# Optimization experiments

Hardware: AMD Instinct MI355X
Metric: run time of the kernel (lower is better)

The kernel has to match this reference:

```python
import jax, jax.numpy as jnp
import numpy as np

# PlatonicConv (graph mode, attention=True, use_key=True): tetrahedron group G=12
G = 12
H_EFF = 2          # num_heads // G = 24 // 12
HEAD_D = 16        # embed_dim_g // H_EFF = (384//12) // 2
GH = G * H_EFF     # 24
IN_C = 384
EMB = 384
OUT_C = 384
N_GRAPHS = 32
NODES_PER_GRAPH = 64
N = N_GRAPHS * NODES_PER_GRAPH   # 2048
SPATIAL = 3


def _fc_edges():
    # fully-connected edges within each graph (batch[src]==batch[dst]), incl. self loops
    n = NODES_PER_GRAPH
    offs = np.arange(N_GRAPHS, dtype=np.int32) * n
    gs, gd = np.meshgrid(np.arange(n, dtype=np.int32), np.arange(n, dtype=np.int32), indexing='ij')
    src = (offs[:, None] + gs.reshape(-1)[None, :]).reshape(-1)
    dst = (offs[:, None] + gd.reshape(-1)[None, :]).reshape(-1)
    return jnp.asarray(src), jnp.asarray(dst)


def setup_inputs() -> dict:
    key = jax.random.key(0)
    ks = jax.random.split(key, 12)
    sw = 1.0 / np.sqrt(IN_C)
    x = jax.random.normal(ks[0], (N, IN_C), jnp.float32)
    pos = jax.random.normal(ks[1], (N, SPATIAL), jnp.float32)
    Wq = jax.random.normal(ks[2], (IN_C, EMB), jnp.float32) * sw
    bq = jnp.zeros((EMB,), jnp.float32)
    Wk = jax.random.normal(ks[3], (IN_C, EMB), jnp.float32) * sw
    bk = jnp.zeros((EMB,), jnp.float32)
    Wv = jax.random.normal(ks[4], (IN_C, EMB), jnp.float32) * sw
    bv = jnp.zeros((EMB,), jnp.float32)
    Wo = jax.random.normal(ks[5], (EMB, OUT_C), jnp.float32) * (1.0 / np.sqrt(EMB))
    bo = jnp.zeros((OUT_C,), jnp.float32)
    # RoPE frequencies: freq_sigma=1.0, random init, per spatial dim / head / half-dim
    rope_freqs = jax.random.normal(ks[6], (SPATIAL, H_EFF, HEAD_D // 2), jnp.float32)
    src, dst = _fc_edges()
    return {"x": x, "pos": pos, "Wq": Wq, "bq": bq, "Wk": Wk, "bk": bk,
            "Wv": Wv, "bv": bv, "Wo": Wo, "bo": bo, "rope_freqs": rope_freqs,
            "src": src, "dst": dst}


def _rope(t, pos, freqs):
    # t: [N, G, H, D]; pos: [N, 3]; freqs: [3, H, D//2]
    theta = jnp.einsum('ns,shf->nhf', pos, freqs)            # [N, H, D/2]
    cos = jnp.cos(theta)[:, None, :, :]                      # broadcast over G
    sin = jnp.sin(theta)[:, None, :, :]
    tr = t.reshape(t.shape[:-1] + (HEAD_D // 2, 2))
    t1, t2 = tr[..., 0], tr[..., 1]
    rot = jnp.stack([t1 * cos - t2 * sin, t1 * sin + t2 * cos], axis=-1)
    return rot.reshape(t.shape)


def reference(x, pos, Wq, bq, Wk, bk, Wv, bv, Wo, bo, rope_freqs, src, dst):
    n = x.shape[0]
    q = (x @ Wq + bq).reshape(n, G, H_EFF, HEAD_D)
    k = (x @ Wk + bk).reshape(n, G, H_EFF, HEAD_D)
    v = (x @ Wv + bv).reshape(n, G, H_EFF, HEAD_D)
    q = _rope(q, pos, rope_freqs)
    k = _rope(k, pos, rope_freqs)
    qf = q.reshape(n, GH, HEAD_D)
    kf = k.reshape(n, GH, HEAD_D)
    vf = v.reshape(n, GH, HEAD_D)
    # gather by edge index
    q_src = qf[src]                                          # [E, GH, D]
    k_dst = kf[dst]
    v_dst = vf[dst]
    scores = jnp.sum(q_src * k_dst, axis=-1) * (HEAD_D ** -0.5)  # [E, GH]
    # scatter softmax over edges grouped by src node (per group-head)
    m = jax.ops.segment_max(scores, src, num_segments=n)     # [N, GH]
    ex = jnp.exp(scores - m[src])
    den = jax.ops.segment_sum(ex, src, num_segments=n)
    a = ex / den[src]                                        # [E, GH]
    out = jax.ops.segment_sum(a[..., None] * v_dst, src, num_segments=n)  # [N, GH, D]
    out = out.reshape(n, GH * HEAD_D)
    return out @ Wo + bo
```

## Files before the change

### kernel.cpp

```cpp
#include <hip/hip_runtime.h>


#define NNODES   2048
#define EMBD     384
#define QKV_LD   1152
#define NGRAPHS  32
#define NPG      64
#define GHEADS   24
#define HDIM     16

typedef __attribute__((ext_vector_type(8))) short short8;
typedef __attribute__((ext_vector_type(4))) float f32x4;

__device__ __forceinline__ short f2bf(float f) {
    unsigned u = __builtin_bit_cast(unsigned, f);
    u += 0x7FFFu + ((u >> 16) & 1u);
    return (short)(u >> 16);
}

__global__ __launch_bounds__(256) void gemm_bias_kernel(
    const float* __restrict__ A, int lda,
    const float* __restrict__ B0, const float* __restrict__ B1,
    const float* __restrict__ B2, int ldb,
    const float* __restrict__ bias0, const float* __restrict__ bias1,
    const float* __restrict__ bias2,
    float* __restrict__ C, int ldc, int K)
{
    __shared__ __align__(16) short As[64 * 40];
    __shared__ __align__(16) short Bs[64 * 40];

    const int tid = threadIdx.x;
    const int m0 = blockIdx.x * 64;
    const int n0 = blockIdx.y * 64;

    const int seg = n0 / 384;
    const float* __restrict__ B    = (seg == 0) ? B0 : (seg == 1) ? B1 : B2;
    const float* __restrict__ bias = (seg == 0) ? bias0 : (seg == 1) ? bias1 : bias2;
    const int nloc = n0 - seg * 384;

    const int r  = tid >> 2;
    const int kq = (tid & 3) * 8;

    const int lane = tid & 63;
    const int w    = tid >> 6;
    const int wr   = (w >> 1) * 32;
    const int wc   = (w & 1) * 32;
    const int fr   = lane & 15;
    const int ko   = (lane >> 4) * 8;

    f32x4 acc[2][2];
    #pragma unroll
    for (int i = 0; i < 2; ++i)
        #pragma unroll
        for (int j = 0; j < 2; ++j)
            acc[i][j] = (f32x4){0.f, 0.f, 0.f, 0.f};

    for (int kt = 0; kt < K; kt += 32) {
        {
            const f32x4* ap = reinterpret_cast<const f32x4*>(
                A + (size_t)(m0 + r) * lda + kt + kq);
            f32x4 a0 = ap[0];
            f32x4 a1 = ap[1];
            short8 av;
            av[0] = f2bf(a0[0]); av[1] = f2bf(a0[1]);
            av[2] = f2bf(a0[2]); av[3] = f2bf(a0[3]);
            av[4] = f2bf(a1[0]); av[5] = f2bf(a1[1]);
            av[6] = f2bf(a1[2]); av[7] = f2bf(a1[3]);
            *reinterpret_cast<short8*>(&As[r * 40 + kq]) = av;
        }
        {
            const float* bp = B + (size_t)(kt + kq) * ldb + nloc + r;
            short8 bv;
            #pragma unroll
            for (int j = 0; j < 8; ++j)
                bv[j] = f2bf(bp[(size_t)j * ldb]);
            *reinterpret_cast<short8*>(&Bs[r * 40 + kq]) = bv;
        }
        __syncthreads();

        short8 af0 = *reinterpret_cast<const short8*>(&As[(wr + fr) * 40 + ko]);
        short8 af1 = *reinterpret_cast<const short8*>(&As[(wr + 16 + fr) * 40 + ko]);
        short8 bf0 = *reinterpret_cast<const short8*>(&Bs[(wc + fr) * 40 + ko]);
        short8 bf1 = *reinterpret_cast<const short8*>(&Bs[(wc + 16 + fr) * 40 + ko]);

        acc[0][0] = __builtin_amdgcn_mfma_f32_16x16x32_bf16(af0, bf0, acc[0][0], 0, 0, 0);
        acc[0][1] = __builtin_amdgcn_mfma_f32_16x16x32_bf16(af0, bf1, acc[0][1], 0, 0, 0);
        acc[1][0] = __builtin_amdgcn_mfma_f32_16x16x32_bf16(af1, bf0, acc[1][0], 0, 0, 0);
        acc[1][1] = __builtin_amdgcn_mfma_f32_16x16x32_bf16(af1, bf1, acc[1][1], 0, 0, 0);
        __syncthreads();
    }

    #pragma unroll
    for (int mi = 0; mi < 2; ++mi) {
        #pragma unroll
        for (int ni = 0; ni < 2; ++ni) {
            const int col  = n0 + wc + ni * 16 + fr;
            const float bv = bias[nloc + wc + ni * 16 + fr];
            const int rowb = m0 + wr + mi * 16 + (lane >> 4) * 4;
            #pragma unroll
            for (int rr = 0; rr < 4; ++rr) {
                C[(size_t)(rowb + rr) * ldc + col] = acc[mi][ni][rr] + bv;
            }
        }
    }
}

__global__ __launch_bounds__(64) void attn_kernel(
    const float* __restrict__ qkv,
    const float* __restrict__ pos,
    const float* __restrict__ freqs,
    float* __restrict__ attn_out)
{
    const int blk  = blockIdx.x;
    const int gr   = blk / GHEADS;
    const int gh   = blk - gr * GHEADS;
    const int h    = gh & 1;
    const int lane = threadIdx.x;
    const int n    = gr * NPG + lane;

    const float* rowq = qkv + (size_t)n * QKV_LD + gh * HDIM;
    const float* rowk = rowq + 384;
    const float* rowv = rowq + 768;

    const float p0 = pos[n * 3 + 0], p1 = pos[n * 3 + 1], p2 = pos[n * 3 + 2];
    float cs[8], sn[8];
    #pragma unroll
    for (int f = 0; f < 8; ++f) {
        const float th = p0 * freqs[h * 8 + f]
                       + p1 * freqs[16 + h * 8 + f]
                       + p2 * freqs[32 + h * 8 + f];
        cs[f] = __cosf(th);
        sn[f] = __sinf(th);
    }

    __shared__ float klds[NPG][HDIM];
    __shared__ float vlds[NPG][HDIM];

    float q[HDIM];
    #pragma unroll
    for (int f = 0; f < 8; ++f) {
        const float q1 = rowq[2 * f], q2 = rowq[2 * f + 1];
        q[2 * f]     = q1 * cs[f] - q2 * sn[f];
        q[2 * f + 1] = q1 * sn[f] + q2 * cs[f];
    }
    #pragma unroll
    for (int f = 0; f < 8; ++f) {
        const float k1 = rowk[2 * f], k2 = rowk[2 * f + 1];
        klds[lane][2 * f]     = k1 * cs[f] - k2 * sn[f];
        klds[lane][2 * f + 1] = k1 * sn[f] + k2 * cs[f];
    }
    #pragma unroll
    for (int d = 0; d < HDIM; ++d)
        vlds[lane][d] = rowv[d];
    __syncthreads();

    float sc[NPG];
    #pragma unroll
    for (int j = 0; j < NPG; ++j) {
        float a = 0.f;
        #pragma unroll
        for (int d = 0; d < HDIM; ++d)
            a += q[d] * klds[j][d];
        sc[j] = a * 0.25f;
    }

    float m = sc[0];
    #pragma unroll
    for (int j = 1; j < NPG; ++j) m = fmaxf(m, sc[j]);

    float den = 0.f;
    #pragma unroll
    for (int j = 0; j < NPG; ++j) {
        sc[j] = __expf(sc[j] - m);
        den += sc[j];
    }

    float o[HDIM];
    #pragma unroll
    for (int d = 0; d < HDIM; ++d) o[d] = 0.f;
    #pragma unroll
    for (int j = 0; j < NPG; ++j) {
        const float p = sc[j];
        #pragma unroll
        for (int d = 0; d < HDIM; ++d)
            o[d] += p * vlds[j][d];
    }

    const float inv = 1.0f / den;
    float* outp = attn_out + (size_t)n * EMBD + gh * HDIM;
    #pragma unroll
    for (int d = 0; d < HDIM; ++d)
        outp[d] = o[d] * inv;
}

extern "C" void kernel_launch(void* const* d_in, const int* in_sizes, int n_in,
                              void* d_out, int out_size, void* d_ws, size_t ws_size,
                              hipStream_t stream) {
    const float* x     = (const float*)d_in[0];
    const float* pos   = (const float*)d_in[1];
    const float* Wq    = (const float*)d_in[2];
    const float* bq    = (const float*)d_in[3];
    const float* Wk    = (const float*)d_in[4];
    const float* bk    = (const float*)d_in[5];
    const float* Wv    = (const float*)d_in[6];
    const float* bv    = (const float*)d_in[7];
    const float* Wo    = (const float*)d_in[8];
    const float* bo    = (const float*)d_in[9];
    const float* rope  = (const float*)d_in[10];

    float* qkv  = (float*)d_ws;
    float* attn = (float*)((char*)d_ws + (size_t)NNODES * QKV_LD * 4);

    {
        dim3 grid(NNODES / 64, QKV_LD / 64);
        gemm_bias_kernel<<<grid, 256, 0, stream>>>(
            x, EMBD, Wq, Wk, Wv, EMBD, bq, bk, bv, qkv, QKV_LD, EMBD);
    }
    {
        attn_kernel<<<NGRAPHS * GHEADS, 64, 0, stream>>>(qkv, pos, rope, attn);
    }
    {
        dim3 grid(NNODES / 64, EMBD / 64);
        gemm_bias_kernel<<<grid, 256, 0, stream>>>(
            attn, EMBD, Wo, Wo, Wo, EMBD, bo, bo, bo, (float*)d_out, EMBD, EMBD);
    }
}
```

Measured before the change: 127.3 us.

## Pre-convert weights and activations to bf16, fuse RoPE into QKV GEMM epilogue

Adds a prep kernel that transposes all four weight matrices into bf16 and converts x to bf16, so the GEMMs load contiguous bf16 rows instead of strided fp32 columns that need per-element conversion. The GEMM now uses a 64-wide K tile with register prefetch of the next tile, and applies RoPE in the epilogue through lane shuffles. The attention kernel drops its RoPE work, uses vectorized loads, and writes bf16 output for the output projection. The price is an extra kernel launch and weight conversion that runs on every call, plus more workspace.

Measured after the change: 109.8 us. 1.16x faster.

```diff
diff --git a/kernel.cpp b/kernel.cpp
--- a/kernel.cpp
+++ b/kernel.cpp
@@ -2,8 +2,8 @@
 
 
 #define NNODES   2048
-#define EMBD     384
-#define QKV_LD   1152
+#define KDIM     384
+#define QKV_N    1152
 #define NGRAPHS  32
 #define NPG      64
 #define GHEADS   24
@@ -18,28 +18,71 @@
     return (short)(u >> 16);
 }
 
-__global__ __launch_bounds__(256) void gemm_bias_kernel(
-    const float* __restrict__ A, int lda,
-    const float* __restrict__ B0, const float* __restrict__ B1,
-    const float* __restrict__ B2, int ldb,
-    const float* __restrict__ bias0, const float* __restrict__ bias1,
-    const float* __restrict__ bias2,
-    float* __restrict__ C, int ldc, int K)
+__global__ __launch_bounds__(256) void prep_kernel(
+    const float* __restrict__ x,
+    const float* __restrict__ Wq, const float* __restrict__ Wk,
+    const float* __restrict__ Wv, const float* __restrict__ Wo,
+    const float* __restrict__ bq, const float* __restrict__ bk,
+    const float* __restrict__ bv,
+    short* __restrict__ WT, short* __restrict__ xb,
+    float* __restrict__ bias_cat)
 {
-    __shared__ __align__(16) short As[64 * 40];
-    __shared__ __align__(16) short Bs[64 * 40];
-
+    const int b   = blockIdx.x;
     const int tid = threadIdx.x;
-    const int m0 = blockIdx.x * 64;
-    const int n0 = blockIdx.y * 64;
-
-    const int seg = n0 / 384;
-    const float* __restrict__ B    = (seg == 0) ? B0 : (seg == 1) ? B1 : B2;
-    const float* __restrict__ bias = (seg == 0) ? bias0 : (seg == 1) ? bias1 : bias2;
-    const int nloc = n0 - seg * 384;
+    if (b < 576) {
+        __shared__ float tile[32][33];
+        const int mat = b / 144;
+        const int t   = b - mat * 144;
+        const int k0  = (t / 12) * 32;
+        const int n0  = (t % 12) * 32;
+        const float* W = (mat == 0) ? Wq : (mat == 1) ? Wk : (mat == 2) ? Wv : Wo;
+        const int cx = tid & 31;
+        const int ty = tid >> 5;
+        #pragma unroll
+        for (int i = 0; i < 4; ++i) {
+            const int rr = ty + 8 * i;
+            tile[rr][cx] = W[(size_t)(k0 + rr) * KDIM + n0 + cx];
+        }
+        __syncthreads();
+        #pragma unroll
+        for (int i = 0; i < 4; ++i) {
+            const int rr = ty + 8 * i;
+            WT[(size_t)(mat * 384 + n0 + rr) * KDIM + k0 + cx] = f2bf(tile[cx][rr]);
+        }
+    } else if (b < 960) {
+        const int idx = ((b - 576) * 256 + tid) * 8;
+        const f32x4* xp = reinterpret_cast<const f32x4*>(x + idx);
+        f32x4 v0 = xp[0], v1 = xp[1];
+        short8 o;
+        o[0] = f2bf(v0[0]); o[1] = f2bf(v0[1]); o[2] = f2bf(v0[2]); o[3] = f2bf(v0[3]);
+        o[4] = f2bf(v1[0]); o[5] = f2bf(v1[1]); o[6] = f2bf(v1[2]); o[7] = f2bf(v1[3]);
+        *reinterpret_cast<short8*>(xb + idx) = o;
+    } else {
+        for (int i = tid; i < QKV_N; i += 256) {
+            const int seg = i / 384;
+            const float* bp = (seg == 0) ? bq : (seg == 1) ? bk : bv;
+            bias_cat[i] = bp[i - seg * 384];
+        }
+    }
+}
+
+__global__ __launch_bounds__(256) void gemm_kernel(
+    const short* __restrict__ A,
+    const short* __restrict__ BT,
+    const float* __restrict__ bias,
+    float* __restrict__ C, int ldc,
+    const float* __restrict__ pos, const float* __restrict__ freqs,
+    int do_rope)
+{
+    __shared__ __align__(16) short As[64 * 72];
+    __shared__ __align__(16) short Bs[64 * 72];
+
+    const int tid = threadIdx.x;
+    const int m0  = blockIdx.x * 64;
+    const int n0  = blockIdx.y * 64;
 
     const int r  = tid >> 2;
-    const int kq = (tid & 3) * 8;
+    const int kq = (tid & 3) * 16;
 
     const int lane = tid & 63;
     const int w    = tid >> 6;
@@ -48,6 +91,19 @@
     const int fr   = lane & 15;
     const int ko   = (lane >> 4) * 8;
 
+    const short* aRow = A  + (size_t)(m0 + r) * KDIM;
+    const short* bRow = BT + (size_t)(n0 + r) * KDIM;
+
+    short8 a0 = *reinterpret_cast<const short8*>(aRow + kq);
+    short8 a1 = *reinterpret_cast<const short8*>(aRow + kq + 8);
+    short8 b0 = *reinterpret_cast<const short8*>(bRow + kq);
+    short8 b1 = *reinterpret_cast<const short8*>(bRow + kq + 8);
+    *reinterpret_cast<short8*>(&As[r * 72 + kq])     = a0;
+    *reinterpret_cast<short8*>(&As[r * 72 + kq + 8]) = a1;
+    *reinterpret_cast<short8*>(&Bs[r * 72 + kq])     = b0;
+    *reinterpret_cast<short8*>(&Bs[r * 72 + kq + 8]) = b1;
+    __syncthreads();
+
     f32x4 acc[2][2];
     #pragma unroll
     for (int i = 0; i < 2; ++i)
@@ -55,112 +111,113 @@
         for (int j = 0; j < 2; ++j)
             acc[i][j] = (f32x4){0.f, 0.f, 0.f, 0.f};
 
-    for (int kt = 0; kt < K; kt += 32) {
-        {
-            const f32x4* ap = reinterpret_cast<const f32x4*>(
-                A + (size_t)(m0 + r) * lda + kt + kq);
-            f32x4 a0 = ap[0];
-            f32x4 a1 = ap[1];
-            short8 av;
-            av[0] = f2bf(a0[0]); av[1] = f2bf(a0[1]);
-            av[2] = f2bf(a0[2]); av[3] = f2bf(a0[3]);
-            av[4] = f2bf(a1[0]); av[5] = f2bf(a1[1]);
-            av[6] = f2bf(a1[2]); av[7] = f2bf(a1[3]);
-            *reinterpret_cast<short8*>(&As[r * 40 + kq]) = av;
-        }
-        {
-            const float* bp = B + (size_t)(kt + kq) * ldb + nloc + r;
-            short8 bv;
+    for (int kt = 0;; kt += 64) {
+        const bool has_next = (kt + 64) < KDIM;
+        short8 na0, na1, nb0, nb1;
+        if (has_next) {
+            na0 = *reinterpret_cast<const short8*>(aRow + kt + 64 + kq);
+            na1 = *reinterpret_cast<const short8*>(aRow + kt + 64 + kq + 8);
+            nb0 = *reinterpret_cast<const short8*>(bRow + kt + 64 + kq);
+            nb1 = *reinterpret_cast<const short8*>(bRow + kt + 64 + kq + 8);
+        }
+        #pragma unroll
+        for (int kk = 0; kk < 64; kk += 32) {
+            short8 af0 = *reinterpret_cast<const short8*>(&As[(wr + fr) * 72 + kk + ko]);
+            short8 af1 = *reinterpret_cast<const short8*>(&As[(wr + 16 + fr) * 72 + kk + ko]);
+            short8 bf0 = *reinterpret_cast<const short8*>(&Bs[(wc + fr) * 72 + kk + ko]);
+            short8 bf1 = *reinterpret_cast<const short8*>(&Bs[(wc + 16 + fr) * 72 + kk + ko]);
+            acc[0][0] = __builtin_amdgcn_mfma_f32_16x16x32_bf16(af0, bf0, acc[0][0], 0, 0, 0);
+            acc[0][1] = __builtin_amdgcn_mfma_f32_16x16x32_bf16(af0, bf1, acc[0][1], 0, 0, 0);
+            acc[1][0] = __builtin_amdgcn_mfma_f32_16x16x32_bf16(af1, bf0, acc[1][0], 0, 0, 0);
+            acc[1][1] = __builtin_amdgcn_mfma_f32_16x16x32_bf16(af1, bf1, acc[1][1], 0, 0, 0);
+        }
+        if (!has_next) break;
+        __syncthreads();
+        *reinterpret_cast<short8*>(&As[r * 72 + kq])     = na0;
+        *reinterpret_cast<short8*>(&As[r * 72 + kq + 8]) = na1;
+        *reinterpret_cast<short8*>(&Bs[r * 72 + kq])     = nb0;
+        *reinterpret_cast<short8*>(&Bs[r * 72 + kq + 8]) = nb1;
+        __syncthreads();
+    }
+
+    const bool rope_wave = do_rope && (n0 < 768);
+    #pragma unroll
+    for (int ni = 0; ni < 2; ++ni) {
+        const int c  = n0 + wc + ni * 16 + fr;
+        const float bv = bias[c];
+        float F0 = 0.f, F1 = 0.f, F2 = 0.f;
+        if (rope_wave) {
+            const int f = fr >> 1;
+            const int h = (c >> 4) & 1;
+            F0 = freqs[h * 8 + f];
+            F1 = freqs[16 + h * 8 + f];
+            F2 = freqs[32 + h * 8 + f];
+        }
+        #pragma unroll
+        for (int mi = 0; mi < 2; ++mi) {
+            const int rowb = m0 + wr + mi * 16 + (lane >> 4) * 4;
+            float v[4];
             #pragma unroll
-            for (int j = 0; j < 8; ++j)
-                bv[j] = f2bf(bp[(size_t)j * ldb]);
-            *reinterpret_cast<short8*>(&Bs[r * 40 + kq]) = bv;
-        }
-        __syncthreads();
-
-        short8 af0 = *reinterpret_cast<const short8*>(&As[(wr + fr) * 40 + ko]);
-        short8 af1 = *reinterpret_cast<const short8*>(&As[(wr + 16 + fr) * 40 + ko]);
-        short8 bf0 = *reinterpret_cast<const short8*>(&Bs[(wc + fr) * 40 + ko]);
-        short8 bf1 = *reinterpret_cast<const short8*>(&Bs[(wc + 16 + fr) * 40 + ko]);
-
-        acc[0][0] = __builtin_amdgcn_mfma_f32_16x16x32_bf16(af0, bf0, acc[0][0], 0, 0, 0);
-        acc[0][1] = __builtin_amdgcn_mfma_f32_16x16x32_bf16(af0, bf1, acc[0][1], 0, 0, 0);
-        acc[1][0] = __builtin_amdgcn_mfma_f32_16x16x32_bf16(af1, bf0, acc[1][0], 0, 0, 0);
-        acc[1][1] = __builtin_amdgcn_mfma_f32_16x16x32_bf16(af1, bf1, acc[1][1], 0, 0, 0);
-        __syncthreads();
-    }
-
-    #pragma unroll
-    for (int mi = 0; mi < 2; ++mi) {
-        #pragma unroll
-        for (int ni = 0; ni < 2; ++ni) {
-            const int col  = n0 + wc + ni * 16 + fr;
-            const float bv = bias[nloc + wc + ni * 16 + fr];
-            const int rowb = m0 + wr + mi * 16 + (lane >> 4) * 4;
+            for (int rr = 0; rr < 4; ++rr)
+                v[rr] = acc[mi][ni][rr] + bv;
+            if (rope_wave) {
+                #pragma unroll
+                for (int rr = 0; rr < 4; ++rr) {
+                    const int row = rowb + rr;
+                    const float th = pos[row * 3] * F0 + pos[row * 3 + 1] * F1
+                                   + pos[row * 3 + 2] * F2;
+                    const float cs = __cosf(th);
+                    const float sn = __sinf(th);
+                    const float other = __shfl_xor(v[rr], 1, 64);
+                    v[rr] = (fr & 1) ? (other * sn + v[rr] * cs)
+                                     : (v[rr] * cs - other * sn);
+                }
+            }
             #pragma unroll
-            for (int rr = 0; rr < 4; ++rr) {
-                C[(size_t)(rowb + rr) * ldc + col] = acc[mi][ni][rr] + bv;
-            }
+            for (int rr = 0; rr < 4; ++rr)
+                C[(size_t)(rowb + rr) * ldc + c] = v[rr];
         }
     }
 }
 
 __global__ __launch_bounds__(64) void attn_kernel(
     const float* __restrict__ qkv,
-    const float* __restrict__ pos,
-    const float* __restrict__ freqs,
-    float* __restrict__ attn_out)
+    short* __restrict__ attn_out)
 {
     const int blk  = blockIdx.x;
     const int gr   = blk / GHEADS;
     const int gh   = blk - gr * GHEADS;
-    const int h    = gh & 1;
     const int lane = threadIdx.x;
     const int n    = gr * NPG + lane;
 
-    const float* rowq = qkv + (size_t)n * QKV_LD + gh * HDIM;
-    const float* rowk = rowq + 384;
-    const float* rowv = rowq + 768;
-
-    const float p0 = pos[n * 3 + 0], p1 = pos[n * 3 + 1], p2 = pos[n * 3 + 2];
-    float cs[8], sn[8];
-    #pragma unroll
-    for (int f = 0; f < 8; ++f) {
-        const float th = p0 * freqs[h * 8 + f]
-                       + p1 * freqs[16 + h * 8 + f]
-                       + p2 * freqs[32 + h * 8 + f];
-        cs[f] = __cosf(th);
-        sn[f] = __sinf(th);
-    }
+    const float* rowq = qkv + (size_t)n * QKV_N + gh * HDIM;
 
     __shared__ float klds[NPG][HDIM];
     __shared__ float vlds[NPG][HDIM];
 
-    float q[HDIM];
-    #pragma unroll
-    for (int f = 0; f < 8; ++f) {
-        const float q1 = rowq[2 * f], q2 = rowq[2 * f + 1];
-        q[2 * f]     = q1 * cs[f] - q2 * sn[f];
-        q[2 * f + 1] = q1 * sn[f] + q2 * cs[f];
-    }
-    #pragma unroll
-    for (int f = 0; f < 8; ++f) {
-        const float k1 = rowk[2 * f], k2 = rowk[2 * f + 1];
-        klds[lane][2 * f]     = k1 * cs[f] - k2 * sn[f];
-        klds[lane][2 * f + 1] = k1 * sn[f] + k2 * cs[f];
-    }
-    #pragma unroll
-    for (int d = 0; d < HDIM; ++d)
-        vlds[lane][d] = rowv[d];
+    f32x4 q[4];
+    #pragma unroll
+    for (int i = 0; i < 4; ++i)
+        q[i] = reinterpret_cast<const f32x4*>(rowq)[i];
+    #pragma unroll
+    for (int i = 0; i < 4; ++i)
+        reinterpret_cast<f32x4*>(&klds[lane][0])[i] =
+            reinterpret_cast<const f32x4*>(rowq + 384)[i];
+    #pragma unroll
+    for (int i = 0; i < 4; ++i)
+        reinterpret_cast<f32x4*>(&vlds[lane][0])[i] =
+            reinterpret_cast<const f32x4*>(rowq + 768)[i];
     __syncthreads();
 
     float sc[NPG];
     #pragma unroll
     for (int j = 0; j < NPG; ++j) {
-        float a = 0.f;
-        #pragma unroll
-        for (int d = 0; d < HDIM; ++d)
-            a += q[d] * klds[j][d];
+        const f32x4* kp = reinterpret_cast<const f32x4*>(&klds[j][0]);
+        f32x4 k0 = kp[0], k1 = kp[1], k2 = kp[2], k3 = kp[3];
+        float a = q[0][0]*k0[0] + q[0][1]*k0[1] + q[0][2]*k0[2] + q[0][3]*k0[3]
+                + q[1][0]*k1[0] + q[1][1]*k1[1] + q[1][2]*k1[2] + q[1][3]*k1[3]
+                + q[2][0]*k2[0] + q[2][1]*k2[1] + q[2][2]*k2[2] + q[2][3]*k2[3]
+                + q[3][0]*k3[0] + q[3][1]*k3[1] + q[3][2]*k3[2] + q[3][3]*k3[3];
         sc[j] = a * 0.25f;
     }
 
@@ -181,47 +238,65 @@
     #pragma unroll
     for (int j = 0; j < NPG; ++j) {
         const float p = sc[j];
-        #pragma unroll
-        for (int d = 0; d < HDIM; ++d)
-            o[d] += p * vlds[j][d];
+        const f32x4* vp = reinterpret_cast<const f32x4*>(&vlds[j][0]);
+        f32x4 v0 = vp[0], v1 = vp[1], v2 = vp[2], v3 = vp[3];
+        #pragma unroll
+        for (int d = 0; d < 4; ++d) {
+            o[d]      += p * v0[d];
+            o[4 + d]  += p * v1[d];
+            o[8 + d]  += p * v2[d];
+            o[12 + d] += p * v3[d];
+        }
     }
 
     const float inv = 1.0f / den;
-    float* outp = attn_out + (size_t)n * EMBD + gh * HDIM;
-    #pragma unroll
-    for (int d = 0; d < HDIM; ++d)
-        outp[d] = o[d] * inv;
+    short8 r0, r1;
+    #pragma unroll
+    for (int d = 0; d < 8; ++d) {
+        r0[d] = f2bf(o[d] * inv);
+        r1[d] = f2bf(o[8 + d] * inv);
+    }
+    short* outp = attn_out + (size_t)n * 384 + gh * HDIM;
+    *reinterpret_cast<short8*>(outp)     = r0;
+    *reinterpret_cast<short8*>(outp + 8) = r1;
 }
 
 extern "C" void kernel_launch(void* const* d_in, const int* in_sizes, int n_in,
                               void* d_out, int out_size, void* d_ws, size_t ws_size,
                               hipStream_t stream) {
-    const float* x     = (const float*)d_in[0];
-    const float* pos   = (const float*)d_in[1];
-    const float* Wq    = (const float*)d_in[2];
-    const float* bq    = (const float*)d_in[3];
-    const float* Wk    = (const float*)d_in[4];
-    const float* bk    = (const float*)d_in[5];
-    const float* Wv    = (const float*)d_in[6];
-    const float* bv    = (const float*)d_in[7];
-    const float* Wo    = (const float*)d_in[8];
-    const float* bo    = (const float*)d_in[9];
-    const float* rope  = (const float*)d_in[10];
-
-    float* qkv  = (float*)d_ws;
-    float* attn = (float*)((char*)d_ws + (size_t)NNODES * QKV_LD * 4);
+    const float* x    = (const float*)d_in[0];
+    const float* pos  = (const float*)d_in[1];
+    const float* Wq   = (const float*)d_in[2];
+    const float* bq   = (const float*)d_in[3];
+    const float* Wk   = (const float*)d_in[4];
+    const float* bk   = (const float*)d_in[5];
+    const float* Wv   = (const float*)d_in[6];
+    const float* bv   = (const float*)d_in[7];
+    const float* Wo   = (const float*)d_in[8];
+    const float* bo   = (const float*)d_in[9];
+    const float* rope = (const float*)d_in[10];
+
+    char* ws = (char*)d_ws;
+    short* WT       = (short*)(ws);
+    short* xb       = (short*)(ws + 1179648);
+    float* bias_cat = (float*)(ws + 2752512);
+    float* qkv      = (float*)(ws + 2757120);
+    short* attn     = (short*)(ws + 12194304);
+
+    prep_kernel<<<961, 256, 0, stream>>>(x, Wq, Wk, Wv, Wo, bq, bk, bv,
+                                         WT, xb, bias_cat);
 
     {
-        dim3 grid(NNODES / 64, QKV_LD / 64);
-        gemm_bias_kernel<<<grid, 256, 0, stream>>>(
-            x, EMBD, Wq, Wk, Wv, EMBD, bq, bk, bv, qkv, QKV_LD, EMBD);
-    }
+        dim3 grid(NNODES / 64, QKV_N / 64);
+        gemm_kernel<<<grid, 256, 0, stream>>>(xb, WT, bias_cat, qkv, QKV_N,
+                                              pos, rope, 1);
+    }
+
+    attn_kernel<<<NGRAPHS * GHEADS, 64, 0, stream>>>(qkv, attn);
+
     {
-        attn_kernel<<<NGRAPHS * GHEADS, 64, 0, stream>>>(qkv, pos, rope, attn);
-    }
-    {
-        dim3 grid(NNODES / 64, EMBD / 64);
-        gemm_bias_kernel<<<grid, 256, 0, stream>>>(
-            attn, EMBD, Wo, Wo, Wo, EMBD, bo, bo, bo, (float*)d_out, EMBD, EMBD);
-    }
-}
+        dim3 grid(NNODES / 64, KDIM / 64);
+        gemm_kernel<<<grid, 256, 0, stream>>>(attn, WT + (size_t)1152 * KDIM, bo,
+                                              (float*)d_out, KDIM, pos, rope, 0);
+    }
+}
```
